# Kernel tuning notes

Measured on AMD Instinct MI355X. Metric: run time of the kernel, lower is better.

The kernel has to match this reference:

```python
import jax, jax.numpy as jnp
import numpy as np

N = 50000          # nodes
E = 800000         # edges (avg degree 16)
IN, HID, OUT = 128, 128, 32
BN_EPS = 1e-5


def gcn_conv(x, W, b, src, dst):
    """PyG GCNConv: D^-1/2 (A+I) D^-1/2 (x @ W) + b, self-loops included."""
    h = x @ W                                                  # [N, out]
    ones = jnp.ones((src.shape[0],), dtype=x.dtype)
    deg = jax.ops.segment_sum(ones, dst, num_segments=N) + 1.0  # in-degree + self-loop
    dis = jax.lax.rsqrt(deg)                                    # deg^-1/2
    norm = dis[src] * dis[dst]                                  # [E]
    msg = h[src] * norm[:, None]                                # gather + scale, [E, out]
    agg = jax.ops.segment_sum(msg, dst, num_segments=N)         # scatter-add
    agg = agg + h * (dis * dis)[:, None]                        # self-loop term (norm = 1/deg_i)
    return agg + b


def bn_relu(h, g, be):
    # BatchNorm1d in training mode: batch statistics over the node dimension
    mu = jnp.mean(h, axis=0)
    var = jnp.mean((h - mu) ** 2, axis=0)  # biased variance, as torch BN
    return jax.nn.relu((h - mu) * jax.lax.rsqrt(var + BN_EPS) * g + be)


def setup_inputs() -> dict:
    key = jax.random.key(0)
    ks = jax.random.split(key, 8)
    x = jax.random.normal(ks[0], (N, IN), dtype=jnp.float32)
    edge_index = jax.random.randint(ks[1], (2, E), 0, N, dtype=jnp.int64)
    W0 = jax.random.normal(ks[2], (IN, HID), dtype=jnp.float32) / np.sqrt(IN)
    W1 = jax.random.normal(ks[3], (HID, HID), dtype=jnp.float32) / np.sqrt(HID)
    W2 = jax.random.normal(ks[4], (HID, OUT), dtype=jnp.float32) / np.sqrt(HID)
    return {
        "x": x, "edge_index": edge_index,
        "W0": W0, "b0": jnp.zeros((HID,), jnp.float32),
        "g0": jnp.ones((HID,), jnp.float32), "be0": jnp.zeros((HID,), jnp.float32),
        "W1": W1, "b1": jnp.zeros((HID,), jnp.float32),
        "g1": jnp.ones((HID,), jnp.float32), "be1": jnp.zeros((HID,), jnp.float32),
        "W2": W2, "b2": jnp.zeros((OUT,), jnp.float32),
    }


def reference(x, edge_index, W0, b0, g0, be0, W1, b1, g1, be1, W2, b2):
    src, dst = edge_index[0], edge_index[1]
    # block 0: conv -> BN -> ReLU -> (dropout: eval, identity) -> residual
    h = bn_relu(gcn_conv(x, W0, b0, src, dst), g0, be0)
    x = h + x  # use_residual, in_channels == hidden, res_proj is None
    # block 1
    h = bn_relu(gcn_conv(x, W1, b1, src, dst), g1, be1)
    x = h + x
    # final conv + log_softmax over classes
    out = gcn_conv(x, W2, b2, src, dst)
    return jax.nn.log_softmax(out, axis=1)
```

## Files before the change

kernel.cpp:

```cpp
#include <hip/hip_runtime.h>
#include <math.h>

#define NN 50000
#define NNP (NN + 1)
#define NE 800000
#define NEP 1150000
#define NBLK 49
#define NBKT 7
#define BCAP 262144

typedef __attribute__((ext_vector_type(8))) short short8;
typedef __attribute__((ext_vector_type(4))) float float4v;

__device__ inline unsigned int f2bf(float f) {
  unsigned int u = __float_as_uint(f);
  return (u + 0x7fffu + ((u >> 16) & 1u)) >> 16;
}
__device__ inline unsigned int pack2bf(float lo, float hi) {
  return f2bf(lo) | (f2bf(hi) << 16);
}
__device__ inline float bflo(unsigned int p) { return __uint_as_float(p << 16); }
__device__ inline float bfhi(unsigned int p) { return __uint_as_float(p & 0xffff0000u); }

__device__ inline void bn_fold(const float* __restrict__ gstat, const float* __restrict__ g,
                               const float* __restrict__ be, float* __restrict__ bnabS, int tid) {
  if (tid < 128) {
    float s = 0.f, q = 0.f;
    #pragma unroll
    for (int r = 0; r < 8; r++) {
      s += gstat[r * 256 + tid];
      q += gstat[r * 256 + 128 + tid];
    }
    const float inv = 1.f / (float)NN;
    float m = s * inv;
    float var = q * inv - m * m;
    float a = rsqrtf(var + 1e-5f) * g[tid];
    bnabS[tid] = a;
    bnabS[128 + tid] = be[tid] - m * a;
  }
}


__global__ __launch_bounds__(256) void k_init(int* __restrict__ deg8, float* __restrict__ gstat,
                                              int* __restrict__ csr, int* __restrict__ binCnt,
                                              const float* __restrict__ W0, const float* __restrict__ W1,
                                              const float* __restrict__ W2,
                                              unsigned short* __restrict__ wt16) {
  int i = blockIdx.x * 256 + threadIdx.x;
  if (i < NEP) csr[i] = NN;
  if (i < 8 * NN) deg8[i] = 0;
  if (i < 4096) gstat[i] = 0.f;
  if (i < NBKT) binCnt[i] = 0;
  if (i < 32768) {
    int w = i >> 14;
    int rem = i & 16383;
    int k = rem >> 7;
    int n = rem & 127;
    const float* W = w ? W1 : W0;
    wt16[w * 16384 + n * 128 + k] = (unsigned short)f2bf(W[k * 128 + n]);
  } else if (i < 36864) {
    int idx = i - 32768;
    int n = idx >> 7;
    int k = idx & 127;
    wt16[32768 + n * 128 + k] = (unsigned short)f2bf(W2[k * 32 + n]);
  }
}


__global__ __launch_bounds__(1024) void k_binA(const int* __restrict__ src, const int* __restrict__ dst,
                                               int* __restrict__ deg8, int* __restrict__ binCnt,
                                               int2* __restrict__ bin) {
  __shared__ int lcnt[NBKT], lbase[NBKT];
  int tid = threadIdx.x;
  if (tid < NBKT) lcnt[tid] = 0;
  __syncthreads();
  int e = blockIdx.x * 1024 + tid;
  bool act = e < NE;
  int d = 0, s = 0, b = 0, rank = 0;
  if (act) {
    d = dst[e]; s = src[e];
    b = d >> 13;
    atomicAdd(&deg8[(e & 7) * NN + d], 1);
    rank = atomicAdd(&lcnt[b], 1);
  }
  __syncthreads();
  if (tid < NBKT && lcnt[tid] > 0) lbase[tid] = atomicAdd(&binCnt[tid], lcnt[tid]);
  __syncthreads();
  if (act) bin[(size_t)b * BCAP + lbase[b] + rank] = make_int2(d, s);
}


__global__ __launch_bounds__(1024) void k_scan1(const int* __restrict__ deg8, int* __restrict__ degtot,
                                                int* __restrict__ excl, int* __restrict__ blksum) {
  __shared__ int smW[16];
  int t = threadIdx.x;
  int i = blockIdx.x * 1024 + t;
  int wv = t >> 6, ln = t & 63;
  int tot = 0;
  if (i < NN) {
    #pragma unroll
    for (int j = 0; j < 8; j++) tot += deg8[j * NN + i];
    degtot[i] = tot;
  }
  int v = (i < NN) ? ((tot + 7) & ~7) : 0;
  int sc = v;
  #pragma unroll
  for (int off = 1; off < 64; off <<= 1) {
    int u = __shfl_up(sc, off);
    if (ln >= off) sc += u;
  }
  if (ln == 63) smW[wv] = sc;
  __syncthreads();
  if (t < 64) {
    int wsum = (t < 16) ? smW[t] : 0;
    int s2 = wsum;
    #pragma unroll
    for (int off = 1; off < 16; off <<= 1) {
      int u = __shfl_up(s2, off);
      if (t >= off) s2 += u;
    }
    if (t < 16) smW[t] = s2 - wsum;
    if (t == 15) blksum[blockIdx.x] = s2;
  }
  __syncthreads();
  if (i < NN) excl[i] = (sc - v) + smW[wv];
}


__global__ __launch_bounds__(256) void k_scan3(int* __restrict__ rowstart, const int* __restrict__ blksum,
                                               const int* __restrict__ degtot, int* __restrict__ cursor,
                                               float* __restrict__ dis,
                                               unsigned short* __restrict__ hs16, float* __restrict__ h2) {
  __shared__ int offS;
  int tid = threadIdx.x;
  int i = blockIdx.x * 256 + tid;
  int myblk = blockIdx.x >> 2;
  if (tid < 64) {
    int bv = (tid < NBLK) ? blksum[tid] : 0;
    int sc = bv;
    #pragma unroll
    for (int off = 1; off < 64; off <<= 1) {
      int u = __shfl_up(sc, off);
      if (tid >= off) sc += u;
    }
    int pre = (myblk > 0) ? __shfl(sc, myblk - 1) : 0;
    int total = __shfl(sc, NBLK - 1);
    if (tid == 0) {
      offS = pre;
      if (blockIdx.x == 0) rowstart[NN] = total;
    }
  }
  __syncthreads();
  int boff = offS;
  if (i < NN) {
    int rs = rowstart[i] + boff;
    rowstart[i] = rs;
    cursor[i] = rs;
    dis[i] = rsqrtf((float)degtot[i] + 1.0f);
  }
  if (i < 64) {
    int slice = i >> 5, c = i & 31;
    ((unsigned int*)(hs16 + (size_t)slice * ((size_t)NNP * 64) + (size_t)NN * 64))[c] = 0u;
  }
  if (i < 32) h2[(size_t)NN * 32 + i] = 0.f;
}


__global__ __launch_bounds__(256) void k_fillB(const int2* __restrict__ bin, const int* __restrict__ binCnt,
                                               int* __restrict__ cursor, int* __restrict__ csr_src) {
  int b = blockIdx.x & 7;
  if (b >= NBKT) return;
  int q = blockIdx.x >> 3;
  int cnt = binCnt[b];
  const int2* __restrict__ B = bin + (size_t)b * BCAP;
  for (int i = q * 256 + threadIdx.x; i < cnt; i += 64 * 256) {
    int2 ds = B[i];
    int p = atomicAdd(&cursor[ds.x], 1);
    csr_src[p] = ds.y;
  }
}


__global__ __launch_bounds__(256) void k_gemm128(const float* __restrict__ X,
                                                 const unsigned short* __restrict__ Wt,
                                                 const float* __restrict__ dis,
                                                 unsigned short* __restrict__ hs16, int M) {
  __shared__ char smem[52224];
  unsigned short* A  = (unsigned short*)smem;
  unsigned short* Bt = (unsigned short*)(smem + 17408);
  float* C = (float*)smem;
  const int tid = threadIdx.x;
  const int row0 = blockIdx.x * 64;

  {
    int c4 = tid & 31;
    #pragma unroll
    for (int i = 0; i < 8; i++) {
      int r = (tid >> 5) + i * 8;
      int gr = row0 + r;
      float4 v = make_float4(0.f, 0.f, 0.f, 0.f);
      if (gr < M) v = *(const float4*)(X + (size_t)gr * 128 + c4 * 4);
      *(uint2*)(A + r * 136 + c4 * 4) = make_uint2(pack2bf(v.x, v.y), pack2bf(v.z, v.w));
    }
  }
  {
    int r = tid >> 1, h = (tid & 1) * 64;
    const uint4* src = (const uint4*)(Wt + r * 128 + h);
    uint4* dst = (uint4*)(Bt + r * 136 + h);
    #pragma unroll
    for (int i = 0; i < 8; i++) dst[i] = src[i];
  }
  __syncthreads();

  const int wv = tid >> 6;
  const int l = tid & 63;
  const int lm = l & 15;
  const int lq = l >> 4;

  float4v acc[8];
  #pragma unroll
  for (int j = 0; j < 8; j++) acc[j] = (float4v)(0.f);

  const unsigned short* Arow = A + (wv * 16 + lm) * 136 + lq * 8;
  #pragma unroll
  for (int ks = 0; ks < 4; ks++) {
    short8 af = *(const short8*)(Arow + ks * 32);
    #pragma unroll
    for (int j = 0; j < 8; j++) {
      short8 bf = *(const short8*)(Bt + (j * 16 + lm) * 136 + lq * 8 + ks * 32);
      acc[j] = __builtin_amdgcn_mfma_f32_16x16x32_bf16(af, bf, acc[j], 0, 0, 0);
    }
  }
  __syncthreads();

  #pragma unroll
  for (int j = 0; j < 8; j++) {
    int col = j * 16 + lm;
    int rbase = wv * 16 + lq * 4;
    #pragma unroll
    for (int r = 0; r < 4; r++) C[(rbase + r) * 132 + col] = acc[j][r];
  }
  __syncthreads();

  {
    #pragma unroll
    for (int i = 0; i < 4; i++) {
      int idx = tid + i * 256;
      int slice = idx >> 9;
      int r = (idx >> 3) & 63;
      int ch = idx & 7;
      int gr = row0 + r;
      if (gr < M) {
        float d = dis[gr];
        const float* cp = C + r * 132 + slice * 64 + ch * 8;
        uint4 u;
        u.x = pack2bf(cp[0] * d, cp[1] * d);
        u.y = pack2bf(cp[2] * d, cp[3] * d);
        u.z = pack2bf(cp[4] * d, cp[5] * d);
        u.w = pack2bf(cp[6] * d, cp[7] * d);
        *(uint4*)(hs16 + (size_t)slice * ((size_t)NNP * 64) + (size_t)gr * 64 + ch * 8) = u;
      }
    }
  }
}


__global__ __launch_bounds__(256) void k_gemm128f(const unsigned short* __restrict__ O16,
                                                  const float* __restrict__ Xin,
                                                  unsigned short* __restrict__ XA16,
                                                  const float* __restrict__ gstat,
                                                  const float* __restrict__ g,
                                                  const float* __restrict__ be,
                                                  const unsigned short* __restrict__ Wt,
                                                  const float* __restrict__ dis,
                                                  unsigned short* __restrict__ hs16, int M) {
  __shared__ char smem[52224];
  __shared__ float bnabS[256];
  unsigned short* A  = (unsigned short*)smem;
  unsigned short* Bt = (unsigned short*)(smem + 17408);
  float* C = (float*)smem;
  const int tid = threadIdx.x;
  const int row0 = blockIdx.x * 64;

  bn_fold(gstat, g, be, bnabS, tid);
  __syncthreads();

  {
    int c = tid & 15;
    float4 alo = *(const float4*)(bnabS + c * 8);
    float4 ahi = *(const float4*)(bnabS + c * 8 + 4);
    float4 clo = *(const float4*)(bnabS + 128 + c * 8);
    float4 chi = *(const float4*)(bnabS + 128 + c * 8 + 4);
    #pragma unroll
    for (int i = 0; i < 4; i++) {
      int r = (tid >> 4) + i * 16;
      int gr = row0 + r;
      uint4 u = make_uint4(0u, 0u, 0u, 0u);
      if (gr < M) {
        uint4 ou = *(const uint4*)(O16 + (size_t)gr * 128 + c * 8);
        float4 xlo = *(const float4*)(Xin + (size_t)gr * 128 + c * 8);
        float4 xhi = *(const float4*)(Xin + (size_t)gr * 128 + c * 8 + 4);
        float v0 = fmaxf(bflo(ou.x) * alo.x + clo.x, 0.f) + xlo.x;
        float v1 = fmaxf(bfhi(ou.x) * alo.y + clo.y, 0.f) + xlo.y;
        float v2 = fmaxf(bflo(ou.y) * alo.z + clo.z, 0.f) + xlo.z;
        float v3 = fmaxf(bfhi(ou.y) * alo.w + clo.w, 0.f) + xlo.w;
        float v4 = fmaxf(bflo(ou.z) * ahi.x + chi.x, 0.f) + xhi.x;
        float v5 = fmaxf(bfhi(ou.z) * ahi.y + chi.y, 0.f) + xhi.y;
        float v6 = fmaxf(bflo(ou.w) * ahi.z + chi.z, 0.f) + xhi.z;
        float v7 = fmaxf(bfhi(ou.w) * ahi.w + chi.w, 0.f) + xhi.w;
        u.x = pack2bf(v0, v1);
        u.y = pack2bf(v2, v3);
        u.z = pack2bf(v4, v5);
        u.w = pack2bf(v6, v7);
        *(uint4*)(XA16 + (size_t)gr * 128 + c * 8) = u;
      }
      *(uint4*)(A + r * 136 + c * 8) = u;
    }
  }
  {
    int r = tid >> 1, h = (tid & 1) * 64;
    const uint4* src = (const uint4*)(Wt + r * 128 + h);
    uint4* dst = (uint4*)(Bt + r * 136 + h);
    #pragma unroll
    for (int i = 0; i < 8; i++) dst[i] = src[i];
  }
  __syncthreads();

  const int wv = tid >> 6;
  const int l = tid & 63;
  const int lm = l & 15;
  const int lq = l >> 4;

  float4v acc[8];
  #pragma unroll
  for (int j = 0; j < 8; j++) acc[j] = (float4v)(0.f);

  const unsigned short* Arow = A + (wv * 16 + lm) * 136 + lq * 8;
  #pragma unroll
  for (int ks = 0; ks < 4; ks++) {
    short8 af = *(const short8*)(Arow + ks * 32);
    #pragma unroll
    for (int j = 0; j < 8; j++) {
      short8 bf = *(const short8*)(Bt + (j * 16 + lm) * 136 + lq * 8 + ks * 32);
      acc[j] = __builtin_amdgcn_mfma_f32_16x16x32_bf16(af, bf, acc[j], 0, 0, 0);
    }
  }
  __syncthreads();

  #pragma unroll
  for (int j = 0; j < 8; j++) {
    int col = j * 16 + lm;
    int rbase = wv * 16 + lq * 4;
    #pragma unroll
    for (int r = 0; r < 4; r++) C[(rbase + r) * 132 + col] = acc[j][r];
  }
  __syncthreads();

  {
    #pragma unroll
    for (int i = 0; i < 4; i++) {
      int idx = tid + i * 256;
      int slice = idx >> 9;
      int r = (idx >> 3) & 63;
      int ch = idx & 7;
      int gr = row0 + r;
      if (gr < M) {
        float d = dis[gr];
        const float* cp = C + r * 132 + slice * 64 + ch * 8;
        uint4 u;
        u.x = pack2bf(cp[0] * d, cp[1] * d);
        u.y = pack2bf(cp[2] * d, cp[3] * d);
        u.z = pack2bf(cp[4] * d, cp[5] * d);
        u.w = pack2bf(cp[6] * d, cp[7] * d);
        *(uint4*)(hs16 + (size_t)slice * ((size_t)NNP * 64) + (size_t)gr * 64 + ch * 8) = u;
      }
    }
  }
}


__global__ __launch_bounds__(256) void k_gemm32mf(const unsigned short* __restrict__ O16,
                                                  const unsigned short* __restrict__ XA16,
                                                  const float* __restrict__ gstat,
                                                  const float* __restrict__ g,
                                                  const float* __restrict__ be,
                                                  const unsigned short* __restrict__ Wt2,
                                                  const float* __restrict__ dis,
                                                  float* __restrict__ H, int M) {
  __shared__ char smem[26112];
  __shared__ float bnabS[256];
  unsigned short* A   = (unsigned short*)smem;
  unsigned short* Bt2 = (unsigned short*)(smem + 17408);
  float* C = (float*)smem;
  const int tid = threadIdx.x;
  const int row0 = blockIdx.x * 64;

  bn_fold(gstat, g, be, bnabS, tid);
  __syncthreads();

  {
    int c = tid & 15;
    float4 alo = *(const float4*)(bnabS + c * 8);
    float4 ahi = *(const float4*)(bnabS + c * 8 + 4);
    float4 clo = *(const float4*)(bnabS + 128 + c * 8);
    float4 chi = *(const float4*)(bnabS + 128 + c * 8 + 4);
    #pragma unroll
    for (int i = 0; i < 4; i++) {
      int r = (tid >> 4) + i * 16;
      int gr = row0 + r;
      uint4 u = make_uint4(0u, 0u, 0u, 0u);
      if (gr < M) {
        uint4 ou = *(const uint4*)(O16 + (size_t)gr * 128 + c * 8);
        uint4 xu = *(const uint4*)(XA16 + (size_t)gr * 128 + c * 8);
        float v0 = fmaxf(bflo(ou.x) * alo.x + clo.x, 0.f) + bflo(xu.x);
        float v1 = fmaxf(bfhi(ou.x) * alo.y + clo.y, 0.f) + bfhi(xu.x);
        float v2 = fmaxf(bflo(ou.y) * alo.z + clo.z, 0.f) + bflo(xu.y);
        float v3 = fmaxf(bfhi(ou.y) * alo.w + clo.w, 0.f) + bfhi(xu.y);
        float v4 = fmaxf(bflo(ou.z) * ahi.x + chi.x, 0.f) + bflo(xu.z);
        float v5 = fmaxf(bfhi(ou.z) * ahi.y + chi.y, 0.f) + bfhi(xu.z);
        float v6 = fmaxf(bflo(ou.w) * ahi.z + chi.z, 0.f) + bflo(xu.w);
        float v7 = fmaxf(bfhi(ou.w) * ahi.w + chi.w, 0.f) + bfhi(xu.w);
        u.x = pack2bf(v0, v1);
        u.y = pack2bf(v2, v3);
        u.z = pack2bf(v4, v5);
        u.w = pack2bf(v6, v7);
      }
      *(uint4*)(A + r * 136 + c * 8) = u;
    }
  }
  {
    int r = tid >> 3, h = (tid & 7) * 16;
    const uint4* src = (const uint4*)(Wt2 + r * 128 + h);
    uint4* dst = (uint4*)(Bt2 + r * 136 + h);
    dst[0] = src[0];
    dst[1] = src[1];
  }
  __syncthreads();

  const int wv = tid >> 6;
  const int l = tid & 63;
  const int lm = l & 15;
  const int lq = l >> 4;

  float4v acc[2];
  acc[0] = (float4v)(0.f);
  acc[1] = (float4v)(0.f);

  const unsigned short* Arow = A + (wv * 16 + lm) * 136 + lq * 8;
  #pragma unroll
  for (int ks = 0; ks < 4; ks++) {
    short8 af = *(const short8*)(Arow + ks * 32);
    #pragma unroll
    for (int j = 0; j < 2; j++) {
      short8 bf = *(const short8*)(Bt2 + (j * 16 + lm) * 136 + lq * 8 + ks * 32);
      acc[j] = __builtin_amdgcn_mfma_f32_16x16x32_bf16(af, bf, acc[j], 0, 0, 0);
    }
  }
  __syncthreads();

  #pragma unroll
  for (int j = 0; j < 2; j++) {
    int col = j * 16 + lm;
    int rbase = wv * 16 + lq * 4;
    #pragma unroll
    for (int r = 0; r < 4; r++) C[(rbase + r) * 36 + col] = acc[j][r];
  }
  __syncthreads();

  {
    #pragma unroll
    for (int i = 0; i < 2; i++) {
      int idx = tid + i * 256;
      int r = idx >> 3;
      int ch = idx & 7;
      int gr = row0 + r;
      if (gr < M) {
        float d = dis[gr];
        const float* cp = C + r * 36 + ch * 4;
        float4 v = make_float4(cp[0] * d, cp[1] * d, cp[2] * d, cp[3] * d);
        *(float4*)(H + (size_t)gr * 32 + ch * 4) = v;
      }
    }
  }
}


__global__ __launch_bounds__(256) void k_agg128s(const unsigned short* __restrict__ Hs,
                                                 const float* __restrict__ dis,
                                                 const int* __restrict__ rowstart,
                                                 const int* __restrict__ csr_src,
                                                 const float* __restrict__ bias,
                                                 unsigned short* __restrict__ out16,
                                                 float* __restrict__ gstat) {
  __shared__ float smS[4][128], smQ[4][128];
  const int tid = threadIdx.x;
  const int wv = tid >> 6;
  const int lane = tid & 63;
  const int node_sub = lane >> 3;
  const int fl = lane & 7;
  const int base = node_sub * 8;
  const int w = blockIdx.x * 32 + wv * 8 + node_sub;
  const bool act = w < NN;
  const unsigned short* __restrict__ S0 = Hs + fl * 8;
  const unsigned short* __restrict__ S1 = Hs + (size_t)NNP * 64 + fl * 8;
  float di = act ? dis[w] : 0.f;
  int e0 = 0, e1 = 0;
  if (act) { e0 = rowstart[w]; e1 = rowstart[w + 1]; }

  float a0[8], a1[8];
  #pragma unroll
  for (int j = 0; j < 8; j++) { a0[j] = 0.f; a1[j] = 0.f; }

  int idxCur = (e0 < e1) ? csr_src[e0 + fl] : 0;
  for (int e = e0; e < e1; e += 8) {
    int cur = idxCur;
    if (e + 8 < e1) idxCur = csr_src[e + 8 + fl];
    int s0 = __shfl(cur, base + 0), s1 = __shfl(cur, base + 1);
    int s2 = __shfl(cur, base + 2), s3 = __shfl(cur, base + 3);
    int s4 = __shfl(cur, base + 4), s5 = __shfl(cur, base + 5);
    int s6 = __shfl(cur, base + 6), s7 = __shfl(cur, base + 7);
    uint4 g0 = *(const uint4*)(S0 + (size_t)s0 * 64);
    uint4 g1 = *(const uint4*)(S0 + (size_t)s1 * 64);
    uint4 g2 = *(const uint4*)(S0 + (size_t)s2 * 64);
    uint4 g3 = *(const uint4*)(S0 + (size_t)s3 * 64);
    uint4 g4 = *(const uint4*)(S0 + (size_t)s4 * 64);
    uint4 g5 = *(const uint4*)(S0 + (size_t)s5 * 64);
    uint4 g6 = *(const uint4*)(S0 + (size_t)s6 * 64);
    uint4 g7 = *(const uint4*)(S0 + (size_t)s7 * 64);
    uint4 h0 = *(const uint4*)(S1 + (size_t)s0 * 64);
    uint4 h1 = *(const uint4*)(S1 + (size_t)s1 * 64);
    uint4 h2 = *(const uint4*)(S1 + (size_t)s2 * 64);
    uint4 h3 = *(const uint4*)(S1 + (size_t)s3 * 64);
    uint4 h4 = *(const uint4*)(S1 + (size_t)s4 * 64);
    uint4 h5 = *(const uint4*)(S1 + (size_t)s5 * 64);
    uint4 h6 = *(const uint4*)(S1 + (size_t)s6 * 64);
    uint4 h7 = *(const uint4*)(S1 + (size_t)s7 * 64);
    a0[0] += ((bflo(g0.x) + bflo(g1.x)) + (bflo(g2.x) + bflo(g3.x))) + ((bflo(g4.x) + bflo(g5.x)) + (bflo(g6.x) + bflo(g7.x)));
    a0[1] += ((bfhi(g0.x) + bfhi(g1.x)) + (bfhi(g2.x) + bfhi(g3.x))) + ((bfhi(g4.x) + bfhi(g5.x)) + (bfhi(g6.x) + bfhi(g7.x)));
    a0[2] += ((bflo(g0.y) + bflo(g1.y)) + (bflo(g2.y) + bflo(g3.y))) + ((bflo(g4.y) + bflo(g5.y)) + (bflo(g6.y) + bflo(g7.y)));
    a0[3] += ((bfhi(g0.y) + bfhi(g1.y)) + (bfhi(g2.y) + bfhi(g3.y))) + ((bfhi(g4.y) + bfhi(g5.y)) + (bfhi(g6.y) + bfhi(g7.y)));
    a0[4] += ((bflo(g0.z) + bflo(g1.z)) + (bflo(g2.z) + bflo(g3.z))) + ((bflo(g4.z) + bflo(g5.z)) + (bflo(g6.z) + bflo(g7.z)));
    a0[5] += ((bfhi(g0.z) + bfhi(g1.z)) + (bfhi(g2.z) + bfhi(g3.z))) + ((bfhi(g4.z) + bfhi(g5.z)) + (bfhi(g6.z) + bfhi(g7.z)));
    a0[6] += ((bflo(g0.w) + bflo(g1.w)) + (bflo(g2.w) + bflo(g3.w))) + ((bflo(g4.w) + bflo(g5.w)) + (bflo(g6.w) + bflo(g7.w)));
    a0[7] += ((bfhi(g0.w) + bfhi(g1.w)) + (bfhi(g2.w) + bfhi(g3.w))) + ((bfhi(g4.w) + bfhi(g5.w)) + (bfhi(g6.w) + bfhi(g7.w)));
    a1[0] += ((bflo(h0.x) + bflo(h1.x)) + (bflo(h2.x) + bflo(h3.x))) + ((bflo(h4.x) + bflo(h5.x)) + (bflo(h6.x) + bflo(h7.x)));
    a1[1] += ((bfhi(h0.x) + bfhi(h1.x)) + (bfhi(h2.x) + bfhi(h3.x))) + ((bfhi(h4.x) + bfhi(h5.x)) + (bfhi(h6.x) + bfhi(h7.x)));
    a1[2] += ((bflo(h0.y) + bflo(h1.y)) + (bflo(h2.y) + bflo(h3.y))) + ((bflo(h4.y) + bflo(h5.y)) + (bflo(h6.y) + bflo(h7.y)));
    a1[3] += ((bfhi(h0.y) + bfhi(h1.y)) + (bfhi(h2.y) + bfhi(h3.y))) + ((bfhi(h4.y) + bfhi(h5.y)) + (bfhi(h6.y) + bfhi(h7.y)));
    a1[4] += ((bflo(h0.z) + bflo(h1.z)) + (bflo(h2.z) + bflo(h3.z))) + ((bflo(h4.z) + bflo(h5.z)) + (bflo(h6.z) + bflo(h7.z)));
    a1[5] += ((bfhi(h0.z) + bfhi(h1.z)) + (bfhi(h2.z) + bfhi(h3.z))) + ((bfhi(h4.z) + bfhi(h5.z)) + (bfhi(h6.z) + bfhi(h7.z)));
    a1[6] += ((bflo(h0.w) + bflo(h1.w)) + (bflo(h2.w) + bflo(h3.w))) + ((bflo(h4.w) + bflo(h5.w)) + (bflo(h6.w) + bflo(h7.w)));
    a1[7] += ((bfhi(h0.w) + bfhi(h1.w)) + (bfhi(h2.w) + bfhi(h3.w))) + ((bfhi(h4.w) + bfhi(h5.w)) + (bfhi(h6.w) + bfhi(h7.w)));
  }

  float rv0[8], rv1[8];
  if (act) {
    uint4 sv0 = *(const uint4*)(S0 + (size_t)w * 64);
    uint4 sv1 = *(const uint4*)(S1 + (size_t)w * 64);
    float se0[8] = { bflo(sv0.x), bfhi(sv0.x), bflo(sv0.y), bfhi(sv0.y),
                     bflo(sv0.z), bfhi(sv0.z), bflo(sv0.w), bfhi(sv0.w) };
    float se1[8] = { bflo(sv1.x), bfhi(sv1.x), bflo(sv1.y), bfhi(sv1.y),
                     bflo(sv1.z), bfhi(sv1.z), bflo(sv1.w), bfhi(sv1.w) };
    #pragma unroll
    for (int j = 0; j < 8; j++) {
      rv0[j] = (a0[j] + se0[j]) * di + bias[fl * 8 + j];
      rv1[j] = (a1[j] + se1[j]) * di + bias[64 + fl * 8 + j];
    }
    uint4 u0, u1;
    u0.x = pack2bf(rv0[0], rv0[1]); u0.y = pack2bf(rv0[2], rv0[3]);
    u0.z = pack2bf(rv0[4], rv0[5]); u0.w = pack2bf(rv0[6], rv0[7]);
    u1.x = pack2bf(rv1[0], rv1[1]); u1.y = pack2bf(rv1[2], rv1[3]);
    u1.z = pack2bf(rv1[4], rv1[5]); u1.w = pack2bf(rv1[6], rv1[7]);
    *(uint4*)(out16 + (size_t)w * 128 + fl * 8)      = u0;
    *(uint4*)(out16 + (size_t)w * 128 + 64 + fl * 8) = u1;
  } else {
    #pragma unroll
    for (int j = 0; j < 8; j++) { rv0[j] = 0.f; rv1[j] = 0.f; }
  }

  float q0[8], q1[8];
  #pragma unroll
  for (int j = 0; j < 8; j++) { q0[j] = rv0[j] * rv0[j]; q1[j] = rv1[j] * rv1[j]; }
  #pragma unroll
  for (int off = 8; off <= 32; off <<= 1) {
    #pragma unroll
    for (int j = 0; j < 8; j++) {
      rv0[j] += __shfl_xor(rv0[j], off);
      q0[j]  += __shfl_xor(q0[j], off);
      rv1[j] += __shfl_xor(rv1[j], off);
      q1[j]  += __shfl_xor(q1[j], off);
    }
  }
  if (node_sub == 0) {
    #pragma unroll
    for (int j = 0; j < 8; j++) {
      smS[wv][fl * 8 + j] = rv0[j];      smQ[wv][fl * 8 + j] = q0[j];
      smS[wv][64 + fl * 8 + j] = rv1[j]; smQ[wv][64 + fl * 8 + j] = q1[j];
    }
  }
  __syncthreads();
  if (tid < 128) {
    float s = (smS[0][tid] + smS[1][tid]) + (smS[2][tid] + smS[3][tid]);
    float q = (smQ[0][tid] + smQ[1][tid]) + (smQ[2][tid] + smQ[3][tid]);
    int rep = blockIdx.x & 7;
    atomicAdd(&gstat[rep * 256 + tid], s);
    atomicAdd(&gstat[rep * 256 + 128 + tid], q);
  }
}


__global__ __launch_bounds__(256) void k_agg32lsm(const float* __restrict__ H2,
                                                  const float* __restrict__ dis,
                                                  const int* __restrict__ rowstart,
                                                  const int* __restrict__ csr_src,
                                                  const float* __restrict__ bias,
                                                  float* __restrict__ out) {
  int wave = (blockIdx.x * 256 + threadIdx.x) >> 6;
  int lane = threadIdx.x & 63;
  int half = lane >> 5;
  int l = lane & 31;
  int hbase = half * 32;
  int w = wave * 2 + half;
  if (w >= NN) return;
  const float* __restrict__ S = H2 + l;
  float di = dis[w];
  int e0 = rowstart[w], e1 = rowstart[w + 1];
  float acc = 0.f;
  for (int e = e0; e < e1; e += 8) {
    int myIdx = csr_src[e + (l & 7)];
    int s0 = __shfl(myIdx, hbase + 0), s1 = __shfl(myIdx, hbase + 1);
    int s2 = __shfl(myIdx, hbase + 2), s3 = __shfl(myIdx, hbase + 3);
    int s4 = __shfl(myIdx, hbase + 4), s5 = __shfl(myIdx, hbase + 5);
    int s6 = __shfl(myIdx, hbase + 6), s7 = __shfl(myIdx, hbase + 7);
    float h0 = S[(size_t)s0 * 32], h1 = S[(size_t)s1 * 32];
    float h2v = S[(size_t)s2 * 32], h3 = S[(size_t)s3 * 32];
    float h4 = S[(size_t)s4 * 32], h5 = S[(size_t)s5 * 32];
    float h6 = S[(size_t)s6 * 32], h7 = S[(size_t)s7 * 32];
    acc += ((h0 + h1) + (h2v + h3)) + ((h4 + h5) + (h6 + h7));
  }
  float v = (acc + S[(size_t)w * 32]) * di + bias[l];
  float m = v;
  #pragma unroll
  for (int off = 16; off >= 1; off >>= 1) m = fmaxf(m, __shfl_xor(m, off));
  float ex = expf(v - m);
  float s = ex;
  #pragma unroll
  for (int off = 16; off >= 1; off >>= 1) s += __shfl_xor(s, off);
  out[(size_t)w * 32 + l] = v - m - logf(s);
}


extern "C" void kernel_launch(void* const* d_in, const int* in_sizes, int n_in,
                              void* d_out, int out_size, void* d_ws, size_t ws_size,
                              hipStream_t stream) {
  const float* x   = (const float*)d_in[0];
  const int*   ei  = (const int*)d_in[1];
  const float* W0  = (const float*)d_in[2];
  const float* b0  = (const float*)d_in[3];
  const float* g0  = (const float*)d_in[4];
  const float* be0 = (const float*)d_in[5];
  const float* W1  = (const float*)d_in[6];
  const float* b1  = (const float*)d_in[7];
  const float* g1  = (const float*)d_in[8];
  const float* be1 = (const float*)d_in[9];
  const float* W2  = (const float*)d_in[10];
  const float* b2  = (const float*)d_in[11];
  float* out = (float*)d_out;
  const int* srcI = ei;
  const int* dstI = ei + NE;

  char* p = (char*)d_ws;
  auto take = [&](size_t bytes) { char* r = p; p += (bytes + 255) & ~(size_t)255; return (void*)r; };
  int*   deg8     = (int*)take((size_t)8 * NN * 4);
  int*   cursor   = (int*)take(NN * 4);
  int*   degtot   = (int*)take(NN * 4);
  int*   rowstart = (int*)take((NN + 1) * 4);
  int*   blksum   = (int*)take(64 * 4);
  int*   binCnt   = (int*)take(8 * 4);
  float* dis      = (float*)take(NN * 4);
  int*   csr      = (int*)take((size_t)NEP * 4);
  int2*  bin      = (int2*)take((size_t)NBKT * BCAP * 8);
  float* gstat    = (float*)take(4096 * 4);
  unsigned short* wt16 = (unsigned short*)take((2 * 16384 + 4096) * 2);
  unsigned short* hs16 = (unsigned short*)take((size_t)NNP * 128 * 2);
  unsigned short* o16  = (unsigned short*)take((size_t)NN * 128 * 2);
  unsigned short* xA16 = (unsigned short*)take((size_t)NN * 128 * 2);
  float* h2       = (float*)take((size_t)NNP * 32 * 4);

  k_init<<<(NEP + 255) / 256, 256, 0, stream>>>(deg8, gstat, csr, binCnt, W0, W1, W2, wt16);
  k_binA<<<(NE + 1023) / 1024, 1024, 0, stream>>>(srcI, dstI, deg8, binCnt, bin);
  k_scan1<<<NBLK, 1024, 0, stream>>>(deg8, degtot, rowstart, blksum);
  k_scan3<<<(NN + 255) / 256, 256, 0, stream>>>(rowstart, blksum, degtot, cursor, dis, hs16, h2);
  k_fillB<<<512, 256, 0, stream>>>(bin, binCnt, cursor, csr);

  const int aggGrid = (NN + 31) / 32;
  const int aggGrid32 = (NN + 7) / 8;

  k_gemm128<<<(NN + 63) / 64, 256, 0, stream>>>(x, wt16, dis, hs16, NN);
  k_agg128s<<<aggGrid, 256, 0, stream>>>(hs16, dis, rowstart, csr, b0, o16, gstat);

  k_gemm128f<<<(NN + 63) / 64, 256, 0, stream>>>(o16, x, xA16, gstat, g0, be0,
                                                 wt16 + 16384, dis, hs16, NN);
  k_agg128s<<<aggGrid, 256, 0, stream>>>(hs16, dis, rowstart, csr, b1, o16, gstat + 2048);

  k_gemm32mf<<<(NN + 63) / 64, 256, 0, stream>>>(o16, xA16, gstat + 2048, g1, be1,
                                                 wt16 + 32768, dis, h2, NN);
  k_agg32lsm<<<aggGrid32, 256, 0, stream>>>(h2, dis, rowstart, csr, b2, out);
}
```

Before: 288.6 us.

## Fuse CSR fill with first GEMM and drop CSR padding initialization

Merges the CSR fill kernel and the first-layer GEMM into one launch, where the first 512 blocks do the atomic CSR fill and the remaining blocks do the GEMM. The two are independent, so they can overlap and one launch is saved. It also stops pre-filling the padded CSR array with the dummy node index. Instead, the aggregation kernels mask entries past each node's true degree to the zero dummy row, which removes a large memset. The cost is an extra degtot load and a compare per edge chunk, and the fused kernel's large shared-memory allocation also applies to the fill blocks, which may limit their occupancy.

After: 284.3 us. About the same (-1.5%).

```diff
diff --git a/kernel.cpp b/kernel.cpp
--- a/kernel.cpp
+++ b/kernel.cpp
@@ -8,6 +8,8 @@
 #define NBLK 49
 #define NBKT 7
 #define BCAP 262144
+#define GEMMBLK 782
+#define FILLBLK 512
 
 typedef __attribute__((ext_vector_type(8))) short short8;
 typedef __attribute__((ext_vector_type(4))) float float4v;
@@ -42,12 +44,11 @@
 
 
 __global__ __launch_bounds__(256) void k_init(int* __restrict__ deg8, float* __restrict__ gstat,
-                                              int* __restrict__ csr, int* __restrict__ binCnt,
+                                              int* __restrict__ binCnt,
                                               const float* __restrict__ W0, const float* __restrict__ W1,
                                               const float* __restrict__ W2,
                                               unsigned short* __restrict__ wt16) {
   int i = blockIdx.x * 256 + threadIdx.x;
-  if (i < NEP) csr[i] = NN;
   if (i < 8 * NN) deg8[i] = 0;
   if (i < 4096) gstat[i] = 0.f;
   if (i < NBKT) binCnt[i] = 0;
@@ -166,31 +167,37 @@
 }
 
 
-__global__ __launch_bounds__(256) void k_fillB(const int2* __restrict__ bin, const int* __restrict__ binCnt,
-                                               int* __restrict__ cursor, int* __restrict__ csr_src) {
-  int b = blockIdx.x & 7;
-  if (b >= NBKT) return;
-  int q = blockIdx.x >> 3;
-  int cnt = binCnt[b];
-  const int2* __restrict__ B = bin + (size_t)b * BCAP;
-  for (int i = q * 256 + threadIdx.x; i < cnt; i += 64 * 256) {
-    int2 ds = B[i];
-    int p = atomicAdd(&cursor[ds.x], 1);
-    csr_src[p] = ds.y;
-  }
-}
-
-
-__global__ __launch_bounds__(256) void k_gemm128(const float* __restrict__ X,
-                                                 const unsigned short* __restrict__ Wt,
-                                                 const float* __restrict__ dis,
-                                                 unsigned short* __restrict__ hs16, int M) {
+__global__ __launch_bounds__(256) void k_fillgemm(const int2* __restrict__ bin,
+                                                  const int* __restrict__ binCnt,
+                                                  int* __restrict__ cursor,
+                                                  int* __restrict__ csr_src,
+                                                  const float* __restrict__ X,
+                                                  const unsigned short* __restrict__ Wt,
+                                                  const float* __restrict__ dis,
+                                                  unsigned short* __restrict__ hs16) {
   __shared__ char smem[52224];
+  const int tid = threadIdx.x;
+
+  if (blockIdx.x < FILLBLK) {
+    int bb = blockIdx.x;
+    int b = bb & 7;
+    if (b >= NBKT) return;
+    int q = bb >> 3;
+    int cnt = binCnt[b];
+    const int2* __restrict__ B = bin + (size_t)b * BCAP;
+    for (int i = q * 256 + tid; i < cnt; i += 64 * 256) {
+      int2 ds = B[i];
+      int p = atomicAdd(&cursor[ds.x], 1);
+      csr_src[p] = ds.y;
+    }
+    return;
+  }
+
   unsigned short* A  = (unsigned short*)smem;
   unsigned short* Bt = (unsigned short*)(smem + 17408);
   float* C = (float*)smem;
-  const int tid = threadIdx.x;
-  const int row0 = blockIdx.x * 64;
+  const int row0 = (blockIdx.x - FILLBLK) * 64;
+  const int M = NN;
 
   {
     int c4 = tid & 31;
@@ -488,6 +495,7 @@
 __global__ __launch_bounds__(256) void k_agg128s(const unsigned short* __restrict__ Hs,
                                                  const float* __restrict__ dis,
                                                  const int* __restrict__ rowstart,
+                                                 const int* __restrict__ degtot,
                                                  const int* __restrict__ csr_src,
                                                  const float* __restrict__ bias,
                                                  unsigned short* __restrict__ out16,
@@ -504,8 +512,8 @@
   const unsigned short* __restrict__ S0 = Hs + fl * 8;
   const unsigned short* __restrict__ S1 = Hs + (size_t)NNP * 64 + fl * 8;
   float di = act ? dis[w] : 0.f;
-  int e0 = 0, e1 = 0;
-  if (act) { e0 = rowstart[w]; e1 = rowstart[w + 1]; }
+  int e0 = 0, e1 = 0, dend = 0;
+  if (act) { e0 = rowstart[w]; e1 = rowstart[w + 1]; dend = e0 + degtot[w]; }
 
   float a0[8], a1[8];
   #pragma unroll
@@ -513,7 +521,7 @@
 
   int idxCur = (e0 < e1) ? csr_src[e0 + fl] : 0;
   for (int e = e0; e < e1; e += 8) {
-    int cur = idxCur;
+    int cur = (e + fl < dend) ? idxCur : (int)NN;
     if (e + 8 < e1) idxCur = csr_src[e + 8 + fl];
     int s0 = __shfl(cur, base + 0), s1 = __shfl(cur, base + 1);
     int s2 = __shfl(cur, base + 2), s3 = __shfl(cur, base + 3);
@@ -612,6 +620,7 @@
 __global__ __launch_bounds__(256) void k_agg32lsm(const float* __restrict__ H2,
                                                   const float* __restrict__ dis,
                                                   const int* __restrict__ rowstart,
+                                                  const int* __restrict__ degtot,
                                                   const int* __restrict__ csr_src,
                                                   const float* __restrict__ bias,
                                                   float* __restrict__ out) {
@@ -625,9 +634,11 @@
   const float* __restrict__ S = H2 + l;
   float di = dis[w];
   int e0 = rowstart[w], e1 = rowstart[w + 1];
+  int dend = e0 + degtot[w];
   float acc = 0.f;
   for (int e = e0; e < e1; e += 8) {
     int myIdx = csr_src[e + (l & 7)];
+    if (e + (l & 7) >= dend) myIdx = NN;
     int s0 = __shfl(myIdx, hbase + 0), s1 = __shfl(myIdx, hbase + 1);
     int s2 = __shfl(myIdx, hbase + 2), s3 = __shfl(myIdx, hbase + 3);
     int s4 = __shfl(myIdx, hbase + 4), s5 = __shfl(myIdx, hbase + 5);
@@ -687,23 +698,22 @@
   unsigned short* xA16 = (unsigned short*)take((size_t)NN * 128 * 2);
   float* h2       = (float*)take((size_t)NNP * 32 * 4);
 
-  k_init<<<(NEP + 255) / 256, 256, 0, stream>>>(deg8, gstat, csr, binCnt, W0, W1, W2, wt16);
+  k_init<<<(8 * NN + 255) / 256, 256, 0, stream>>>(deg8, gstat, binCnt, W0, W1, W2, wt16);
   k_binA<<<(NE + 1023) / 1024, 1024, 0, stream>>>(srcI, dstI, deg8, binCnt, bin);
   k_scan1<<<NBLK, 1024, 0, stream>>>(deg8, degtot, rowstart, blksum);
   k_scan3<<<(NN + 255) / 256, 256, 0, stream>>>(rowstart, blksum, degtot, cursor, dis, hs16, h2);
-  k_fillB<<<512, 256, 0, stream>>>(bin, binCnt, cursor, csr);
 
   const int aggGrid = (NN + 31) / 32;
   const int aggGrid32 = (NN + 7) / 8;
 
-  k_gemm128<<<(NN + 63) / 64, 256, 0, stream>>>(x, wt16, dis, hs16, NN);
-  k_agg128s<<<aggGrid, 256, 0, stream>>>(hs16, dis, rowstart, csr, b0, o16, gstat);
+  k_fillgemm<<<FILLBLK + GEMMBLK, 256, 0, stream>>>(bin, binCnt, cursor, csr, x, wt16, dis, hs16);
+  k_agg128s<<<aggGrid, 256, 0, stream>>>(hs16, dis, rowstart, degtot, csr, b0, o16, gstat);
 
   k_gemm128f<<<(NN + 63) / 64, 256, 0, stream>>>(o16, x, xA16, gstat, g0, be0,
                                                  wt16 + 16384, dis, hs16, NN);
-  k_agg128s<<<aggGrid, 256, 0, stream>>>(hs16, dis, rowstart, csr, b1, o16, gstat + 2048);
+  k_agg128s<<<aggGrid, 256, 0, stream>>>(hs16, dis, rowstart, degtot, csr, b1, o16, gstat + 2048);
 
   k_gemm32mf<<<(NN + 63) / 64, 256, 0, stream>>>(o16, xA16, gstat + 2048, g1, be1,
                                                  wt16 + 32768, dis, h2, NN);
-  k_agg32lsm<<<aggGrid32, 256, 0, stream>>>(h2, dis, rowstart, csr, b2, out);
-}
+  k_agg32lsm<<<aggGrid32, 256, 0, stream>>>(h2, dis, rowstart, degtot, csr, b2, out);
+}
```
